# Optimization experiments

Measured on AMD Instinct MI355X. Metric: run time of the kernel, lower is better.

The kernel has to match this reference:

```python
import jax, jax.numpy as jnp
import numpy as np

N = 50000
E = 800000
NFEAT = 128
NHID = 32
HEADS = 8
NCLASS = 40


def _gat_conv(x, src, dst, W, att_src, att_dst, bias, concat):
    # x: [N, Fin]; W: [Fin, H*C]; att_*: [H, C]; bias: [H*C] or [C]
    n = x.shape[0]
    H, C = att_src.shape
    h = (x @ W).reshape(n, H, C)                      # [N,H,C]
    a_src = (h * att_src[None]).sum(-1)               # [N,H]
    a_dst = (h * att_dst[None]).sum(-1)               # [N,H]
    e = jax.nn.leaky_relu(a_src[src] + a_dst[dst], 0.2)  # [E,H]
    # edge softmax over incoming edges of each dst node
    m = jax.ops.segment_max(e, dst, num_segments=n)   # [N,H]
    e = jnp.exp(e - m[dst])
    s = jax.ops.segment_sum(e, dst, num_segments=n)   # [N,H]
    alpha = e / (s[dst] + 1e-16)                      # [E,H]
    msg = h[src] * alpha[:, :, None]                  # [E,H,C]
    out = jax.ops.segment_sum(msg, dst, num_segments=n)  # [N,H,C]
    if concat:
        out = out.reshape(n, H * C)
    else:
        out = out.mean(axis=1)
    return out + bias


def setup_inputs() -> dict:
    key = jax.random.key(0)
    ks = jax.random.split(key, 10)
    x = jax.random.normal(ks[0], (N, NFEAT), dtype=jnp.float32)
    edge_index = jax.random.randint(ks[1], (2, E), 0, N, dtype=jnp.int64)
    sc = 1.0 / np.sqrt(NFEAT)
    W1 = jax.random.uniform(ks[2], (NFEAT, HEADS * NHID), jnp.float32, -sc, sc)
    a1_src = jax.random.uniform(ks[3], (HEADS, NHID), jnp.float32, -sc, sc)
    a1_dst = jax.random.uniform(ks[4], (HEADS, NHID), jnp.float32, -sc, sc)
    b1 = jnp.zeros((HEADS * NHID,), jnp.float32)
    sc2 = 1.0 / np.sqrt(HEADS * NHID)
    W2 = jax.random.uniform(ks[5], (HEADS * NHID, NCLASS), jnp.float32, -sc2, sc2)
    a2_src = jax.random.uniform(ks[6], (1, NCLASS), jnp.float32, -sc2, sc2)
    a2_dst = jax.random.uniform(ks[7], (1, NCLASS), jnp.float32, -sc2, sc2)
    b2 = jnp.zeros((NCLASS,), jnp.float32)
    return {"x": x, "edge_index": edge_index, "W1": W1, "a1_src": a1_src,
            "a1_dst": a1_dst, "b1": b1, "W2": W2, "a2_src": a2_src,
            "a2_dst": a2_dst, "b2": b2}


def reference(x, edge_index, W1, a1_src, a1_dst, b1, W2, a2_src, a2_dst, b2):
    n = x.shape[0]
    loop = jnp.arange(n, dtype=edge_index.dtype)
    src = jnp.concatenate([edge_index[0], loop])  # add self-loops (PyG default)
    dst = jnp.concatenate([edge_index[1], loop])
    # dropout layers are identity in eval mode
    h = jax.nn.elu(_gat_conv(x, src, dst, W1, a1_src, a1_dst, b1, concat=True))
    out = _gat_conv(h, src, dst, W2, a2_src, a2_dst, b2, concat=False)
    return jax.nn.log_softmax(out, axis=1)
```

## Files before the change

kernel.cpp:

```cpp
#include <hip/hip_runtime.h>
#include <math.h>

#define NFEAT  128
#define HC     256
#define HEADS  8
#define NHID   32
#define NCLASS 40

typedef unsigned int  uint;
typedef unsigned short ushort;
typedef unsigned char uchar;

typedef __attribute__((ext_vector_type(8))) short bf16x8;
typedef __attribute__((ext_vector_type(4))) float f32x4;

union U8 { uint4 u; bf16x8 v; };

__device__ __forceinline__ uint f2bf1(float f) {
    uint b = __float_as_uint(f);
    b += 0x7FFFu + ((b >> 16) & 1u);
    return b >> 16;
}
__device__ __forceinline__ uint packbf(float lo, float hi) {
    return f2bf1(lo) | (f2bf1(hi) << 16);
}
__device__ __forceinline__ float bflo(uint u) { return __uint_as_float(u << 16); }
__device__ __forceinline__ float bfhi(uint u) { return __uint_as_float(u & 0xFFFF0000u); }

__device__ __forceinline__ uchar f2fp8(float v) {
    return (uchar)(__builtin_amdgcn_cvt_pk_fp8_f32(v, v, 0, false) & 0xFF);
}
__device__ __forceinline__ float fp8tof(uint byte) {
    auto v2 = __builtin_amdgcn_cvt_pk_f32_fp8((int)byte, false);
    return v2[0];
}


#define HU 4
__global__ void k_hist(const int* __restrict__ dst, int E, int* deg,
                       int* __restrict__ rank) {
    int tid = blockIdx.x * 256 + threadIdx.x;
    int stride = gridDim.x * 256;
#pragma unroll
    for (int j = 0; j < HU; ++j) {
        int i = tid + j * stride;
        if (i < E) rank[i] = atomicAdd(&deg[dst[i]], 1);
    }
}

__global__ void k_blocksum(const int* __restrict__ deg, int n, int* bsum) {
    __shared__ int lds[256];
    int b = blockIdx.x, t = threadIdx.x;
    int i = b * 256 + t;
    lds[t] = (i < n) ? deg[i] + 1 : 0;
    __syncthreads();
    for (int off = 128; off >= 1; off >>= 1) {
        if (t < off) lds[t] += lds[t + off];
        __syncthreads();
    }
    if (t == 0) bsum[b] = lds[0];
}

__global__ void k_mkptr(const int* __restrict__ deg, const int* __restrict__ bsum,
                        int n, int* ptr) {
    __shared__ int lds[256];
    __shared__ int base_s;
    int b = blockIdx.x, t = threadIdx.x;
    int p = 0;
    for (int i = t; i < b; i += 256) p += bsum[i];
    lds[t] = p;
    __syncthreads();
    for (int off = 128; off >= 1; off >>= 1) {
        if (t < off) lds[t] += lds[t + off];
        __syncthreads();
    }
    if (t == 0) base_s = lds[0];
    __syncthreads();
    int i = b * 256 + t;
    int v = (i < n) ? deg[i] + 1 : 0;
    lds[t] = v;
    __syncthreads();
    for (int off = 1; off < 256; off <<= 1) {
        int u = (t >= off) ? lds[t - off] : 0;
        __syncthreads();
        lds[t] += u;
        __syncthreads();
    }
    int excl = lds[t] - v + base_s;
    if (i < n) {
        ptr[i] = excl;
        if (i == n - 1) ptr[n] = excl + v;
    }
}

#define SU 4
__global__ void k_scatter(const int* __restrict__ srcE, const int* __restrict__ dstE,
                          const int* __restrict__ rank, const int* __restrict__ ptr,
                          int E, int n, int* __restrict__ srcs) {
    int tid = blockIdx.x * 256 + threadIdx.x;
    int stride = gridDim.x * 256;
    int tot = E + n;
#pragma unroll
    for (int j = 0; j < SU; ++j) {
        int i = tid + j * stride;
        if (i >= tot) continue;
        if (i < E) {
            int d = dstE[i];
            srcs[ptr[d] + rank[i]] = srcE[i];
        } else {
            int v = i - E;
            srcs[ptr[v + 1] - 1] = v;
        }
    }
}

__global__ __launch_bounds__(256)
void k_prep(const float* __restrict__ W1,
            const float* __restrict__ attS, const float* __restrict__ attD,
            const float* __restrict__ W2,
            const float* __restrict__ a2sw, const float* __restrict__ a2dw,
            ushort* __restrict__ Wb1, ushort* __restrict__ Wb2) {
    int blk = blockIdx.x;
    int t = threadIdx.x;
    float f[8];
    if (blk < 17) {
        int g = blk * 256 + t;
        int lane = g & 63;
        int step = (g >> 6) & 3;
        int tile = g >> 8;
        int k0 = step * 32 + (lane >> 4) * 8;
        if (tile < 16) {
            int ncol = tile * 16 + (lane & 15);
#pragma unroll
            for (int j = 0; j < 8; ++j) f[j] = W1[(size_t)(k0 + j) * HC + ncol];
        } else {
            int cc = lane & 15;
            int h = cc & 7;
            const float* av = (cc < 8) ? attS : attD;
#pragma unroll
            for (int j = 0; j < 8; ++j) {
                const float* wr = W1 + (size_t)(k0 + j) * HC + h * 32;
                float s = 0.f;
#pragma unroll
                for (int c = 0; c < 32; ++c) s += wr[c] * av[h * 32 + c];
                f[j] = s;
            }
        }
        uint4 o;
        o.x = packbf(f[0], f[1]);
        o.y = packbf(f[2], f[3]);
        o.z = packbf(f[4], f[5]);
        o.w = packbf(f[6], f[7]);
        *(uint4*)(Wb1 + (size_t)g * 8) = o;
    } else {
        int g = (blk - 17) * 256 + t;
        if (g >= 3 * 8 * 64) return;
        int lane = g & 63;
        int ks = (g >> 6) & 7;
        int nt = g >> 9;
        int cc = lane & 15;
        int ncol = nt * 16 + cc;
        int k0 = ks * 32 + (lane >> 4) * 8;
        if (ncol < NCLASS) {
#pragma unroll
            for (int j = 0; j < 8; ++j) f[j] = W2[(size_t)(k0 + j) * NCLASS + ncol];
        } else if (ncol <= 41) {
            const float* av = (ncol == 40) ? a2sw : a2dw;
#pragma unroll
            for (int j = 0; j < 8; ++j) {
                const float* wr = W2 + (size_t)(k0 + j) * NCLASS;
                float s = 0.f;
#pragma unroll
                for (int c = 0; c < NCLASS; ++c) s += wr[c] * av[c];
                f[j] = s;
            }
        } else {
#pragma unroll
            for (int j = 0; j < 8; ++j) f[j] = 0.f;
        }
        uint4 o;
        o.x = packbf(f[0], f[1]);
        o.y = packbf(f[2], f[3]);
        o.z = packbf(f[4], f[5]);
        o.w = packbf(f[6], f[7]);
        *(uint4*)(Wb2 + (size_t)g * 8) = o;
    }
}

__global__ __launch_bounds__(256)
void k_gemm1(const float* __restrict__ x,
             const ushort* __restrict__ Wb,
             int n, uchar* __restrict__ h1f8,
             float* __restrict__ a1x) {
    __shared__ uint Xs[64 * 68];
    int t = threadIdx.x;
    int lane = t & 63;
    int w = t >> 6;
    int n0 = blockIdx.x * 64;

#pragma unroll
    for (int j = 0; j < 8; ++j) {
        int f4 = t + j * 256;
        int node = f4 >> 5;
        int k4 = (f4 & 31) * 4;
        int gn = n0 + node;
        float4 v = make_float4(0.f, 0.f, 0.f, 0.f);
        if (gn < n) v = *(const float4*)(x + (size_t)gn * NFEAT + k4);
        uint2 pk;
        pk.x = packbf(v.x, v.y);
        pk.y = packbf(v.z, v.w);
        *(uint2*)(Xs + node * 68 + (k4 >> 1)) = pk;
    }
    __syncthreads();

    int m = lane & 15;
    int q4 = (lane >> 4) * 4;
    bf16x8 Af[4];
#pragma unroll
    for (int ks = 0; ks < 4; ++ks) {
        U8 a;
        a.u = *(const uint4*)(Xs + (w * 16 + m) * 68 + ks * 16 + q4);
        Af[ks] = a.v;
    }
    __syncthreads();

    f32x4 acc[17];
#pragma unroll
    for (int i = 0; i < 17; ++i) acc[i] = (f32x4){0.f, 0.f, 0.f, 0.f};

    const bf16x8* Bf = (const bf16x8*)Wb;
#pragma unroll
    for (int ks = 0; ks < 4; ++ks) {
#pragma unroll
        for (int nt = 0; nt < 17; ++nt) {
            bf16x8 bv = Bf[(size_t)(nt * 4 + ks) * 64 + lane];
            acc[nt] = __builtin_amdgcn_mfma_f32_16x16x32_bf16(Af[ks], bv, acc[nt], 0, 0, 0);
        }
    }

    int cc = lane & 15;
    int r0 = (lane >> 4) * 4;

#pragma unroll
    for (int r = 0; r < 4; ++r) {
        int gn = n0 + w * 16 + r0 + r;
        if (gn < n) a1x[(size_t)gn * 16 + cc] = acc[16][r];
    }

    uchar* CsB = (uchar*)Xs;
#pragma unroll
    for (int nt = 0; nt < 16; ++nt) {
#pragma unroll
        for (int r = 0; r < 4; ++r)
            CsB[(w * 16 + r0 + r) * 272 + nt * 16 + cc] = f2fp8(acc[nt][r]);
    }
    __syncthreads();

    int node_local = t >> 2;
    int q = t & 3;
    int gn = n0 + node_local;
    if (gn < n) {
        const uchar* crow = CsB + node_local * 272 + q * 64;
        uchar* hp = h1f8 + (size_t)gn * HC + q * 64;
#pragma unroll
        for (int i = 0; i < 4; ++i)
            *(uint4*)(hp + i * 16) = *(const uint4*)(crow + i * 16);
    }
}

__global__ __launch_bounds__(256)
void k_agg1(const uint* __restrict__ h1u, const float* __restrict__ a1x,
            const float* __restrict__ b1,
            const int* __restrict__ ptr, const int* __restrict__ srcs,
            int wbase, int wend, ushort* __restrict__ hgb) {
    int wid = wbase + blockIdx.x * 4 + (threadIdx.x >> 6);
    if (wid >= wend) return;
    int lane = threadIdx.x & 63;
    int h = lane >> 3;
    float adn = a1x[(size_t)wid * 16 + 8 + h];
    int beg = __builtin_amdgcn_readfirstlane(ptr[wid]);
    int end = __builtin_amdgcn_readfirstlane(ptr[wid + 1]);
    float m = -INFINITY, s = 0.f;
    float4 acc = make_float4(0.f, 0.f, 0.f, 0.f);

    int i = beg;
    for (; i + 8 <= end; i += 8) {
        int sn[8];
#pragma unroll
        for (int j = 0; j < 8; ++j) sn[j] = __builtin_amdgcn_readfirstlane(srcs[i + j]);
        float av[8];
        uint hv[8];
#pragma unroll
        for (int j = 0; j < 8; ++j) av[j] = a1x[(size_t)sn[j] * 16 + h];
#pragma unroll
        for (int j = 0; j < 8; ++j)
            hv[j] = h1u[(size_t)sn[j] * 64 + lane];
        float e[8];
#pragma unroll
        for (int j = 0; j < 8; ++j) {
            float a = av[j] + adn;
            e[j] = (a > 0.f) ? a : 0.2f * a;
        }
        float mn = m;
#pragma unroll
        for (int j = 0; j < 8; ++j) mn = fmaxf(mn, e[j]);
        float corr = __expf(m - mn);
        float p[8];
#pragma unroll
        for (int j = 0; j < 8; ++j) p[j] = __expf(e[j] - mn);
        float ps = 0.f;
#pragma unroll
        for (int j = 0; j < 8; ++j) ps += p[j];
        s = s * corr + ps;
        float cx = acc.x * corr, cy = acc.y * corr, cz = acc.z * corr, cw = acc.w * corr;
#pragma unroll
        for (int j = 0; j < 8; ++j) {
            auto lo = __builtin_amdgcn_cvt_pk_f32_fp8((int)hv[j], false);
            auto hi = __builtin_amdgcn_cvt_pk_f32_fp8((int)hv[j], true);
            cx += p[j] * lo[0];
            cy += p[j] * lo[1];
            cz += p[j] * hi[0];
            cw += p[j] * hi[1];
        }
        acc = make_float4(cx, cy, cz, cw);
        m = mn;
    }
    if (i < end) {
        int sn[8];
        bool val[8];
#pragma unroll
        for (int j = 0; j < 8; ++j) {
            int idx = i + j;
            val[j] = idx < end;
            sn[j] = __builtin_amdgcn_readfirstlane(srcs[val[j] ? idx : end - 1]);
        }
        float av[8];
        uint hv[8];
#pragma unroll
        for (int j = 0; j < 8; ++j) av[j] = a1x[(size_t)sn[j] * 16 + h];
#pragma unroll
        for (int j = 0; j < 8; ++j)
            hv[j] = h1u[(size_t)sn[j] * 64 + lane];
        float e[8];
#pragma unroll
        for (int j = 0; j < 8; ++j) {
            float a = av[j] + adn;
            e[j] = val[j] ? ((a > 0.f) ? a : 0.2f * a) : -INFINITY;
        }
        float mn = m;
#pragma unroll
        for (int j = 0; j < 8; ++j) mn = fmaxf(mn, e[j]);
        float corr = __expf(m - mn);
        float p[8];
#pragma unroll
        for (int j = 0; j < 8; ++j) p[j] = __expf(e[j] - mn);
        float ps = 0.f;
#pragma unroll
        for (int j = 0; j < 8; ++j) ps += p[j];
        s = s * corr + ps;
        float cx = acc.x * corr, cy = acc.y * corr, cz = acc.z * corr, cw = acc.w * corr;
#pragma unroll
        for (int j = 0; j < 8; ++j) {
            auto lo = __builtin_amdgcn_cvt_pk_f32_fp8((int)hv[j], false);
            auto hi = __builtin_amdgcn_cvt_pk_f32_fp8((int)hv[j], true);
            cx += p[j] * lo[0];
            cy += p[j] * lo[1];
            cz += p[j] * hi[0];
            cw += p[j] * hi[1];
        }
        acc = make_float4(cx, cy, cz, cw);
        m = mn;
    }

    float inv = 1.f / (s + 1e-16f);
    float4 bv = *(const float4*)(b1 + lane * 4);
    float4 o;
    o.x = acc.x * inv + bv.x;
    o.y = acc.y * inv + bv.y;
    o.z = acc.z * inv + bv.z;
    o.w = acc.w * inv + bv.w;
    o.x = (o.x > 0.f) ? o.x : (__expf(o.x) - 1.f);
    o.y = (o.y > 0.f) ? o.y : (__expf(o.y) - 1.f);
    o.z = (o.z > 0.f) ? o.z : (__expf(o.z) - 1.f);
    o.w = (o.w > 0.f) ? o.w : (__expf(o.w) - 1.f);
    uint2 ov;
    ov.x = packbf(o.x, o.y);
    ov.y = packbf(o.z, o.w);
    *(uint2*)(hgb + (size_t)wid * HC + lane * 4) = ov;
}

__global__ __launch_bounds__(256)
void k_gemm2(const ushort* __restrict__ hgb, const ushort* __restrict__ Wb2,
             int n, uchar* __restrict__ h2f8,
             float* __restrict__ a2s, float* __restrict__ a2d) {
    __shared__ uint Xs[64 * 132];
    int t = threadIdx.x;
    int lane = t & 63;
    int w = t >> 6;
    int n0 = blockIdx.x * 64;

#pragma unroll
    for (int j = 0; j < 8; ++j) {
        int g = t + j * 256;
        int node = g >> 5;
        int u4 = g & 31;
        int gn = n0 + node;
        uint4 v = make_uint4(0u, 0u, 0u, 0u);
        if (gn < n) v = *(const uint4*)(hgb + (size_t)gn * HC + u4 * 8);
        *(uint4*)(Xs + node * 132 + u4 * 4) = v;
    }
    __syncthreads();

    int m = lane & 15;
    int q4 = (lane >> 4) * 4;
    bf16x8 Af[8];
#pragma unroll
    for (int ks = 0; ks < 8; ++ks) {
        U8 a;
        a.u = *(const uint4*)(Xs + (w * 16 + m) * 132 + ks * 16 + q4);
        Af[ks] = a.v;
    }
    __syncthreads();

    f32x4 acc[3];
#pragma unroll
    for (int i = 0; i < 3; ++i) acc[i] = (f32x4){0.f, 0.f, 0.f, 0.f};

    const bf16x8* Bf = (const bf16x8*)Wb2;
#pragma unroll
    for (int ks = 0; ks < 8; ++ks) {
#pragma unroll
        for (int nt = 0; nt < 3; ++nt) {
            bf16x8 bv = Bf[(size_t)(nt * 8 + ks) * 64 + lane];
            acc[nt] = __builtin_amdgcn_mfma_f32_16x16x32_bf16(Af[ks], bv, acc[nt], 0, 0, 0);
        }
    }

    int cc = lane & 15;
    int r0 = (lane >> 4) * 4;

#pragma unroll
    for (int r = 0; r < 4; ++r) {
        int gn = n0 + w * 16 + r0 + r;
        if (gn < n) {
            if (cc == 8) a2s[gn] = acc[2][r];
            if (cc == 9) a2d[gn] = acc[2][r];
        }
    }

    uchar* CsB = (uchar*)Xs;
#pragma unroll
    for (int nt = 0; nt < 3; ++nt) {
#pragma unroll
        for (int r = 0; r < 4; ++r)
            CsB[(w * 16 + r0 + r) * 64 + nt * 16 + cc] = f2fp8(acc[nt][r]);
    }
    __syncthreads();

    int node_local = t >> 2;
    int q = t & 3;
    int gn = n0 + node_local;
    if (gn < n)
        *(uint4*)(h2f8 + (size_t)gn * 64 + q * 16) =
            *(const uint4*)(CsB + node_local * 64 + q * 16);
}

__global__ __launch_bounds__(256)
void k_agg2(const uchar* __restrict__ h2f8, const float* __restrict__ a2s,
            const float* __restrict__ a2d, const float* __restrict__ b2,
            const int* __restrict__ ptr, const int* __restrict__ srcs,
            int n, float* __restrict__ out) {
    int wid = blockIdx.x * 4 + (threadIdx.x >> 6);
    if (wid >= n) return;
    int lane = threadIdx.x & 63;
    bool live = lane < NCLASS;
    int col = live ? lane : 0;
    float adn = a2d[wid];
    int beg = __builtin_amdgcn_readfirstlane(ptr[wid]);
    int end = __builtin_amdgcn_readfirstlane(ptr[wid + 1]);
    float m = -INFINITY, s = 0.f, acc = 0.f;

    int i = beg;
    for (; i + 8 <= end; i += 8) {
        int sn[8];
#pragma unroll
        for (int j = 0; j < 8; ++j) sn[j] = __builtin_amdgcn_readfirstlane(srcs[i + j]);
        float av[8];
        uint hb[8];
#pragma unroll
        for (int j = 0; j < 8; ++j) av[j] = a2s[sn[j]];
#pragma unroll
        for (int j = 0; j < 8; ++j)
            hb[j] = h2f8[(size_t)sn[j] * 64 + col];
        float e[8];
#pragma unroll
        for (int j = 0; j < 8; ++j) {
            float a = av[j] + adn;
            e[j] = (a > 0.f) ? a : 0.2f * a;
        }
        float mn = m;
#pragma unroll
        for (int j = 0; j < 8; ++j) mn = fmaxf(mn, e[j]);
        float corr = __expf(m - mn);
        float p[8];
#pragma unroll
        for (int j = 0; j < 8; ++j) p[j] = __expf(e[j] - mn);
        float ps = 0.f, pa = 0.f;
#pragma unroll
        for (int j = 0; j < 8; ++j) { ps += p[j]; pa += p[j] * fp8tof(hb[j]); }
        s = s * corr + ps;
        acc = acc * corr + pa;
        m = mn;
    }
    if (i < end) {
        int sn[8];
        bool val[8];
#pragma unroll
        for (int j = 0; j < 8; ++j) {
            int idx = i + j;
            val[j] = idx < end;
            sn[j] = __builtin_amdgcn_readfirstlane(srcs[val[j] ? idx : end - 1]);
        }
        float av[8];
        uint hb[8];
#pragma unroll
        for (int j = 0; j < 8; ++j) av[j] = a2s[sn[j]];
#pragma unroll
        for (int j = 0; j < 8; ++j)
            hb[j] = h2f8[(size_t)sn[j] * 64 + col];
        float e[8];
#pragma unroll
        for (int j = 0; j < 8; ++j) {
            float a = av[j] + adn;
            e[j] = val[j] ? ((a > 0.f) ? a : 0.2f * a) : -INFINITY;
        }
        float mn = m;
#pragma unroll
        for (int j = 0; j < 8; ++j) mn = fmaxf(mn, e[j]);
        float corr = __expf(m - mn);
        float p[8];
#pragma unroll
        for (int j = 0; j < 8; ++j) p[j] = __expf(e[j] - mn);
        float ps = 0.f, pa = 0.f;
#pragma unroll
        for (int j = 0; j < 8; ++j) { ps += p[j]; pa += p[j] * fp8tof(hb[j]); }
        s = s * corr + ps;
        acc = acc * corr + pa;
        m = mn;
    }

    float val0 = acc / (s + 1e-16f) + (live ? b2[lane] : 0.f);
    float vmax = live ? val0 : -INFINITY;
#pragma unroll
    for (int msk = 1; msk < 64; msk <<= 1) vmax = fmaxf(vmax, __shfl_xor(vmax, msk, 64));
    float ex = live ? __expf(val0 - vmax) : 0.f;
#pragma unroll
    for (int msk = 1; msk < 64; msk <<= 1) ex += __shfl_xor(ex, msk, 64);
    float res = val0 - vmax - __logf(ex);
    if (live) out[(size_t)wid * NCLASS + lane] = res;
}

extern "C" void kernel_launch(void* const* d_in, const int* in_sizes, int n_in,
                              void* d_out, int out_size, void* d_ws, size_t ws_size,
                              hipStream_t stream) {
    const float* x    = (const float*)d_in[0];
    const int*   ei   = (const int*)  d_in[1];
    const float* W1   = (const float*)d_in[2];
    const float* attS = (const float*)d_in[3];
    const float* attD = (const float*)d_in[4];
    const float* b1   = (const float*)d_in[5];
    const float* W2   = (const float*)d_in[6];
    const float* a2sw = (const float*)d_in[7];
    const float* a2dw = (const float*)d_in[8];
    const float* b2   = (const float*)d_in[9];

    int n = in_sizes[0] / NFEAT;
    int E = in_sizes[1] / 2;
    const int* srcE = ei;
    const int* dstE = ei + E;
    int nb = (n + 255) / 256;
    int mblocks = (n + 63) / 64;

    char* p = (char*)d_ws;
    auto alloc = [&](size_t bytes) {
        char* r = p;
        p += (bytes + 255) & ~(size_t)255;
        return r;
    };
    uchar*  h1f8 = (uchar*)alloc((size_t)n * HC);
    ushort* hgb  = (ushort*)alloc((size_t)n * HC * 2);
    uchar*  h2f8 = (uchar*)alloc((size_t)n * 64);
    ushort* Wb1  = (ushort*)alloc((size_t)17 * 4 * 64 * 8 * 2);
    ushort* Wb2  = (ushort*)alloc((size_t)3 * 8 * 64 * 8 * 2);
    float* a1x = (float*)alloc((size_t)n * 16 * 4);
    float* a2s = (float*)alloc((size_t)n * 4);
    float* a2d = (float*)alloc((size_t)n * 4);
    int* deg  = (int*)alloc((size_t)n * 4);
    int* rank = (int*)alloc((size_t)E * 4);
    int* bsum = (int*)alloc((size_t)nb * 4);
    int* ptr  = (int*)alloc((size_t)(n + 1) * 4);
    int* srcs = (int*)alloc((size_t)(E + n) * 4);

    int tot = E + n;
    hipMemsetAsync(deg, 0, (size_t)n * 4, stream);
    k_hist<<<(E + 256 * HU - 1) / (256 * HU), 256, 0, stream>>>(dstE, E, deg, rank);
    k_blocksum<<<nb, 256, 0, stream>>>(deg, n, bsum);
    k_mkptr<<<nb, 256, 0, stream>>>(deg, bsum, n, ptr);
    k_scatter<<<(tot + 256 * SU - 1) / (256 * SU), 256, 0, stream>>>(
        srcE, dstE, rank, ptr, E, n, srcs);

    k_prep<<<23, 256, 0, stream>>>(W1, attS, attD, W2, a2sw, a2dw, Wb1, Wb2);
    k_gemm1<<<mblocks, 256, 0, stream>>>(x, Wb1, n, h1f8, a1x);

    int half = (n + 1) / 2;
    k_agg1<<<(half + 3) / 4, 256, 0, stream>>>((const uint*)h1f8, a1x, b1,
                                               ptr, srcs, 0, half, hgb);
    k_agg1<<<(n - half + 3) / 4, 256, 0, stream>>>((const uint*)h1f8, a1x, b1,
                                                   ptr, srcs, half, n, hgb);

    k_gemm2<<<(n + 63) / 64, 256, 0, stream>>>(hgb, Wb2, n, h2f8, a2s, a2d);
    k_agg2<<<(n + 3) / 4, 256, 0, stream>>>(h2f8, a2s, a2d, b2, ptr, srcs, n, (float*)d_out);
}
```

Baseline: 276.7 us.

## Fuse histogram with weight prep and pack layer-2 attention scalars into fp8 rows

Merges the degree-histogram kernel and the weight-prep kernel into one launch by giving the first blocks the prep work and the rest the atomics, with the per-thread histogram unroll doubled. In layer 2, the per-node source and destination attention logits are stored as floats inside the padding of each 64-byte fp8 feature row instead of separate arrays. k_agg2 then reads them from the same cache line as the gathered features. This saves one launch and the separate random gathers of a2s, at the cost of mixing float data into the fp8 buffer and a fused kernel with uneven block work.

```diff
diff --git a/kernel.cpp b/kernel.cpp
--- a/kernel.cpp
+++ b/kernel.cpp
@@ -36,92 +36,28 @@
 }
 
 
-#define HU 4
-__global__ void k_hist(const int* __restrict__ dst, int E, int* deg,
-                       int* __restrict__ rank) {
-    int tid = blockIdx.x * 256 + threadIdx.x;
-    int stride = gridDim.x * 256;
-#pragma unroll
-    for (int j = 0; j < HU; ++j) {
-        int i = tid + j * stride;
-        if (i < E) rank[i] = atomicAdd(&deg[dst[i]], 1);
-    }
-}
-
-__global__ void k_blocksum(const int* __restrict__ deg, int n, int* bsum) {
-    __shared__ int lds[256];
-    int b = blockIdx.x, t = threadIdx.x;
-    int i = b * 256 + t;
-    lds[t] = (i < n) ? deg[i] + 1 : 0;
-    __syncthreads();
-    for (int off = 128; off >= 1; off >>= 1) {
-        if (t < off) lds[t] += lds[t + off];
-        __syncthreads();
-    }
-    if (t == 0) bsum[b] = lds[0];
-}
-
-__global__ void k_mkptr(const int* __restrict__ deg, const int* __restrict__ bsum,
-                        int n, int* ptr) {
-    __shared__ int lds[256];
-    __shared__ int base_s;
-    int b = blockIdx.x, t = threadIdx.x;
-    int p = 0;
-    for (int i = t; i < b; i += 256) p += bsum[i];
-    lds[t] = p;
-    __syncthreads();
-    for (int off = 128; off >= 1; off >>= 1) {
-        if (t < off) lds[t] += lds[t + off];
-        __syncthreads();
-    }
-    if (t == 0) base_s = lds[0];
-    __syncthreads();
-    int i = b * 256 + t;
-    int v = (i < n) ? deg[i] + 1 : 0;
-    lds[t] = v;
-    __syncthreads();
-    for (int off = 1; off < 256; off <<= 1) {
-        int u = (t >= off) ? lds[t - off] : 0;
-        __syncthreads();
-        lds[t] += u;
-        __syncthreads();
-    }
-    int excl = lds[t] - v + base_s;
-    if (i < n) {
-        ptr[i] = excl;
-        if (i == n - 1) ptr[n] = excl + v;
-    }
-}
-
-#define SU 4
-__global__ void k_scatter(const int* __restrict__ srcE, const int* __restrict__ dstE,
-                          const int* __restrict__ rank, const int* __restrict__ ptr,
-                          int E, int n, int* __restrict__ srcs) {
-    int tid = blockIdx.x * 256 + threadIdx.x;
-    int stride = gridDim.x * 256;
-    int tot = E + n;
-#pragma unroll
-    for (int j = 0; j < SU; ++j) {
-        int i = tid + j * stride;
-        if (i >= tot) continue;
-        if (i < E) {
-            int d = dstE[i];
-            srcs[ptr[d] + rank[i]] = srcE[i];
-        } else {
-            int v = i - E;
-            srcs[ptr[v + 1] - 1] = v;
-        }
-    }
-}
-
+#define HU 8
+#define PREPB 23
 __global__ __launch_bounds__(256)
-void k_prep(const float* __restrict__ W1,
-            const float* __restrict__ attS, const float* __restrict__ attD,
-            const float* __restrict__ W2,
-            const float* __restrict__ a2sw, const float* __restrict__ a2dw,
-            ushort* __restrict__ Wb1, ushort* __restrict__ Wb2) {
+void k_hist_prep(const int* __restrict__ dst, int E, int* deg,
+                 int* __restrict__ rank,
+                 const float* __restrict__ W1,
+                 const float* __restrict__ attS, const float* __restrict__ attD,
+                 const float* __restrict__ W2,
+                 const float* __restrict__ a2sw, const float* __restrict__ a2dw,
+                 ushort* __restrict__ Wb1, ushort* __restrict__ Wb2) {
     int blk = blockIdx.x;
     int t = threadIdx.x;
+    if (blk >= PREPB) {
+        int tid = (blk - PREPB) * 256 + t;
+        int stride = (gridDim.x - PREPB) * 256;
+#pragma unroll
+        for (int j = 0; j < HU; ++j) {
+            int i = tid + j * stride;
+            if (i < E) rank[i] = atomicAdd(&deg[dst[i]], 1);
+        }
+        return;
+    }
     float f[8];
     if (blk < 17) {
         int g = blk * 256 + t;
@@ -187,6 +123,72 @@
     }
 }
 
+__global__ void k_blocksum(const int* __restrict__ deg, int n, int* bsum) {
+    __shared__ int lds[256];
+    int b = blockIdx.x, t = threadIdx.x;
+    int i = b * 256 + t;
+    lds[t] = (i < n) ? deg[i] + 1 : 0;
+    __syncthreads();
+    for (int off = 128; off >= 1; off >>= 1) {
+        if (t < off) lds[t] += lds[t + off];
+        __syncthreads();
+    }
+    if (t == 0) bsum[b] = lds[0];
+}
+
+__global__ void k_mkptr(const int* __restrict__ deg, const int* __restrict__ bsum,
+                        int n, int* ptr) {
+    __shared__ int lds[256];
+    __shared__ int base_s;
+    int b = blockIdx.x, t = threadIdx.x;
+    int p = 0;
+    for (int i = t; i < b; i += 256) p += bsum[i];
+    lds[t] = p;
+    __syncthreads();
+    for (int off = 128; off >= 1; off >>= 1) {
+        if (t < off) lds[t] += lds[t + off];
+        __syncthreads();
+    }
+    if (t == 0) base_s = lds[0];
+    __syncthreads();
+    int i = b * 256 + t;
+    int v = (i < n) ? deg[i] + 1 : 0;
+    lds[t] = v;
+    __syncthreads();
+    for (int off = 1; off < 256; off <<= 1) {
+        int u = (t >= off) ? lds[t - off] : 0;
+        __syncthreads();
+        lds[t] += u;
+        __syncthreads();
+    }
+    int excl = lds[t] - v + base_s;
+    if (i < n) {
+        ptr[i] = excl;
+        if (i == n - 1) ptr[n] = excl + v;
+    }
+}
+
+#define SU 4
+__global__ void k_scatter(const int* __restrict__ srcE, const int* __restrict__ dstE,
+                          const int* __restrict__ rank, const int* __restrict__ ptr,
+                          int E, int n, int* __restrict__ srcs) {
+    int tid = blockIdx.x * 256 + threadIdx.x;
+    int stride = gridDim.x * 256;
+    int tot = E + n;
+#pragma unroll
+    for (int j = 0; j < SU; ++j) {
+        int i = tid + j * stride;
+        if (i >= tot) continue;
+        if (i < E) {
+            int d = dstE[i];
+            srcs[ptr[d] + rank[i]] = srcE[i];
+        } else {
+            int v = i - E;
+            srcs[ptr[v + 1] - 1] = v;
+        }
+    }
+}
+
 __global__ __launch_bounds__(256)
 void k_gemm1(const float* __restrict__ x,
              const ushort* __restrict__ Wb,
@@ -391,8 +393,7 @@
 
 __global__ __launch_bounds__(256)
 void k_gemm2(const ushort* __restrict__ hgb, const ushort* __restrict__ Wb2,
-             int n, uchar* __restrict__ h2f8,
-             float* __restrict__ a2s, float* __restrict__ a2d) {
+             int n, uchar* __restrict__ h2f8) {
     __shared__ uint Xs[64 * 132];
     int t = threadIdx.x;
     int lane = t & 63;
@@ -439,21 +440,23 @@
     int cc = lane & 15;
     int r0 = (lane >> 4) * 4;
 
-#pragma unroll
-    for (int r = 0; r < 4; ++r) {
-        int gn = n0 + w * 16 + r0 + r;
-        if (gn < n) {
-            if (cc == 8) a2s[gn] = acc[2][r];
-            if (cc == 9) a2d[gn] = acc[2][r];
-        }
-    }
-
     uchar* CsB = (uchar*)Xs;
 #pragma unroll
-    for (int nt = 0; nt < 3; ++nt) {
+    for (int nt = 0; nt < 2; ++nt) {
 #pragma unroll
         for (int r = 0; r < 4; ++r)
             CsB[(w * 16 + r0 + r) * 64 + nt * 16 + cc] = f2fp8(acc[nt][r]);
+    }
+#pragma unroll
+    for (int r = 0; r < 4; ++r) {
+        int row = (w * 16 + r0 + r) * 64;
+        if (cc < 8)       CsB[row + 32 + cc] = f2fp8(acc[2][r]);
+        else if (cc == 8) *(float*)(CsB + row + 40) = acc[2][r];
+        else if (cc == 9) *(float*)(CsB + row + 44) = acc[2][r];
+        else if (cc == 10) *(uint*)(CsB + row + 48) = 0u;
+        else if (cc == 11) *(uint*)(CsB + row + 52) = 0u;
+        else if (cc == 12) *(uint*)(CsB + row + 56) = 0u;
+        else if (cc == 13) *(uint*)(CsB + row + 60) = 0u;
     }
     __syncthreads();
 
@@ -466,8 +469,7 @@
 }
 
 __global__ __launch_bounds__(256)
-void k_agg2(const uchar* __restrict__ h2f8, const float* __restrict__ a2s,
-            const float* __restrict__ a2d, const float* __restrict__ b2,
+void k_agg2(const uchar* __restrict__ h2f8, const float* __restrict__ b2,
             const int* __restrict__ ptr, const int* __restrict__ srcs,
             int n, float* __restrict__ out) {
     int wid = blockIdx.x * 4 + (threadIdx.x >> 6);
@@ -475,7 +477,7 @@
     int lane = threadIdx.x & 63;
     bool live = lane < NCLASS;
     int col = live ? lane : 0;
-    float adn = a2d[wid];
+    float adn = *(const float*)(h2f8 + (size_t)wid * 64 + 44);
     int beg = __builtin_amdgcn_readfirstlane(ptr[wid]);
     int end = __builtin_amdgcn_readfirstlane(ptr[wid + 1]);
     float m = -INFINITY, s = 0.f, acc = 0.f;
@@ -488,7 +490,8 @@
         float av[8];
         uint hb[8];
 #pragma unroll
-        for (int j = 0; j < 8; ++j) av[j] = a2s[sn[j]];
+        for (int j = 0; j < 8; ++j)
+            av[j] = *(const float*)(h2f8 + (size_t)sn[j] * 64 + 40);
 #pragma unroll
         for (int j = 0; j < 8; ++j)
             hb[j] = h2f8[(size_t)sn[j] * 64 + col];
@@ -524,7 +527,8 @@
         float av[8];
         uint hb[8];
 #pragma unroll
-        for (int j = 0; j < 8; ++j) av[j] = a2s[sn[j]];
+        for (int j = 0; j < 8; ++j)
+            av[j] = *(const float*)(h2f8 + (size_t)sn[j] * 64 + 40);
 #pragma unroll
         for (int j = 0; j < 8; ++j)
             hb[j] = h2f8[(size_t)sn[j] * 64 + col];
@@ -593,8 +597,6 @@
     ushort* Wb1  = (ushort*)alloc((size_t)17 * 4 * 64 * 8 * 2);
     ushort* Wb2  = (ushort*)alloc((size_t)3 * 8 * 64 * 8 * 2);
     float* a1x = (float*)alloc((size_t)n * 16 * 4);
-    float* a2s = (float*)alloc((size_t)n * 4);
-    float* a2d = (float*)alloc((size_t)n * 4);
     int* deg  = (int*)alloc((size_t)n * 4);
     int* rank = (int*)alloc((size_t)E * 4);
     int* bsum = (int*)alloc((size_t)nb * 4);
@@ -602,14 +604,16 @@
     int* srcs = (int*)alloc((size_t)(E + n) * 4);
 
     int tot = E + n;
+    int histb = (E + 256 * HU - 1) / (256 * HU);
     hipMemsetAsync(deg, 0, (size_t)n * 4, stream);
-    k_hist<<<(E + 256 * HU - 1) / (256 * HU), 256, 0, stream>>>(dstE, E, deg, rank);
+    k_hist_prep<<<PREPB + histb, 256, 0, stream>>>(dstE, E, deg, rank,
+                                                   W1, attS, attD, W2, a2sw, a2dw,
+                                                   Wb1, Wb2);
     k_blocksum<<<nb, 256, 0, stream>>>(deg, n, bsum);
     k_mkptr<<<nb, 256, 0, stream>>>(deg, bsum, n, ptr);
     k_scatter<<<(tot + 256 * SU - 1) / (256 * SU), 256, 0, stream>>>(
         srcE, dstE, rank, ptr, E, n, srcs);
 
-    k_prep<<<23, 256, 0, stream>>>(W1, attS, attD, W2, a2sw, a2dw, Wb1, Wb2);
     k_gemm1<<<mblocks, 256, 0, stream>>>(x, Wb1, n, h1f8, a1x);
 
     int half = (n + 1) / 2;
@@ -618,6 +622,6 @@
     k_agg1<<<(n - half + 3) / 4, 256, 0, stream>>>((const uint*)h1f8, a1x, b1,
                                                    ptr, srcs, half, n, hgb);
 
-    k_gemm2<<<(n + 63) / 64, 256, 0, stream>>>(hgb, Wb2, n, h2f8, a2s, a2d);
-    k_agg2<<<(n + 3) / 4, 256, 0, stream>>>(h2f8, a2s, a2d, b2, ptr, srcs, n, (float*)d_out);
-}
+    k_gemm2<<<(n + 63) / 64, 256, 0, stream>>>(hgb, Wb2, n, h2f8);
+    k_agg2<<<(n + 3) / 4, 256, 0, stream>>>(h2f8, b2, ptr, srcs, n, (float*)d_out);
+}
```

New measurement: 264.1 us. 4.6% less time.
